# Kernel optimization log

Hardware: AMD Instinct MI355X
Metric: run time of the kernel (lower is better)

## Reference

```python
import jax, jax.numpy as jnp
import numpy as np

# ---- static config (matches init_kwargs) ----
B, N, DIM = 1, 2048, 1024
H, KVH, D = 16, 8, 64
GQ = H // KVH                 # grouped queries per kv head
WS = 64                       # sliding window size (causal, exact)
CBS, STRIDE = 32, 16          # compress block size / sliding stride
SEL_BLK, NSEL, NMEM = 32, 4, 1
NCB = N // STRIDE             # num compressed blocks (128)
NFB = N // SEL_BLK            # num fine blocks (64)
NCPF = SEL_BLK // STRIDE      # compressed blocks per fine block (2)
HID = CBS * D                 # compress MLP hidden (expand factor 1.0)
SCALE = D ** -0.5
THETA = 10000.0
NEG = -jnp.finfo(jnp.float32).max


def setup_inputs():
    key = jax.random.key(0)
    ks = jax.random.split(key, 16)
    s = 0.02
    r = lambda i, shape: jax.random.normal(ks[i], shape, jnp.float32) * s
    return {
        "inp": jax.random.normal(ks[0], (B, N, DIM), jnp.float32),
        "norm_g": jnp.ones((DIM,), jnp.float32),
        "Wqkv": r(1, (DIM, (H + 2 * KVH) * D)),
        "mem_kv": r(2, (2, KVH, NMEM, D)),
        "k_pos": r(3, (KVH, CBS, D)),
        "v_pos": r(4, (KVH, CBS, D)),
        "kW1": r(5, (CBS * D, HID)), "kb1": jnp.zeros((HID,), jnp.float32),
        "kW2": r(6, (HID, D)), "kb2": jnp.zeros((D,), jnp.float32),
        "vW1": r(7, (CBS * D, HID)), "vb1": jnp.zeros((HID,), jnp.float32),
        "vW2": r(8, (HID, D)), "vb2": jnp.zeros((D,), jnp.float32),
        "combW": r(9, (DIM, 3 * H)),
        "combB": jnp.tile(jnp.array([-2.0, -2.0, 2.0], jnp.float32), H),
        "Wout": r(10, (H * D, DIM)),
    }


def _rope(t):
    # lucidrains rotary-embedding-torch: interleaved adjacent-pair rotation
    inv_freq = 1.0 / (THETA ** (jnp.arange(0, D, 2, dtype=jnp.float32) / D))
    ang = jnp.arange(N, dtype=jnp.float32)[:, None] * inv_freq        # [N, D/2]
    cos = jnp.repeat(jnp.cos(ang), 2, axis=-1)                        # [N, D]
    sin = jnp.repeat(jnp.sin(ang), 2, axis=-1)
    t2 = t.reshape(*t.shape[:-1], D // 2, 2)
    rot = jnp.stack([-t2[..., 1], t2[..., 0]], axis=-1).reshape(t.shape)
    return t * cos + rot * sin


def _forward(inp, norm_g, Wqkv, mem_kv, k_pos, v_pos,
             kW1, kb1, kW2, kb2, vW1, vb1, vW2, vb2,
             combW, combB, Wout):
    # RMSNorm
    x = inp * jax.lax.rsqrt(jnp.mean(inp * inp, -1, keepdims=True)
                            + jnp.finfo(inp.dtype).eps) * norm_g
    qkv = x @ Wqkv
    q, k, v = jnp.split(qkv, [H * D, H * D + KVH * D], axis=-1)
    q = q.reshape(B, N, H, D).transpose(0, 2, 1, 3)      # b h n d
    k = k.reshape(B, N, KVH, D).transpose(0, 2, 1, 3)    # b kvh n d
    v = v.reshape(B, N, KVH, D).transpose(0, 2, 1, 3)

    # ---- compressed branch (overlapping windows, left zero pad) ----
    overlap = CBS - STRIDE
    kp = jnp.pad(k, ((0, 0), (0, 0), (overlap, 0), (0, 0)))
    vp = jnp.pad(v, ((0, 0), (0, 0), (overlap, 0), (0, 0)))
    widx = jnp.arange(NCB)[:, None] * STRIDE + jnp.arange(CBS)[None, :]  # [NCB, CBS]
    kw = kp[:, :, widx] + k_pos[None, :, None]   # b kvh w cbs d
    vw = vp[:, :, widx] + v_pos[None, :, None]

    def cmlp(t, W1, b1, W2, b2):
        t = t.reshape(B, KVH, NCB, CBS * D)
        return jax.nn.relu(t @ W1 + b1) @ W2 + b2       # b kvh w d

    ck = cmlp(kw, kW1, kb1, kW2, kb2)
    cv = cmlp(vw, vW1, vb1, vW2, vb2)
    ck = jnp.concatenate([jnp.broadcast_to(mem_kv[0], (B, KVH, NMEM, D)), ck], 2)
    cv = jnp.concatenate([jnp.broadcast_to(mem_kv[1], (B, KVH, NMEM, D)), cv], 2)

    qg = q.reshape(B, KVH, GQ, N, D)
    csim = jnp.einsum('bhgid,bhjd->bhgij', qg, ck) * SCALE   # no mask (cmask=None)
    cattn = jax.nn.softmax(csim, -1)
    cout = jnp.einsum('bhgij,bhjd->bhgid', cattn, cv).reshape(B, H, N, D)

    # rotary AFTER compressed attention (as in source)
    rq, rk = _rope(q), _rope(k)

    # ---- importance scores -> top-k fine block selection ----
    imp = csim[..., NMEM:].mean(2)                          # b kvh n NCB (share grouped q)
    imp = imp.reshape(B, KVH, N, NFB, NCPF).mean(-1)        # mean-pool to fine blocks
    q_blk = jnp.arange(N) // SEL_BLK
    diag = q_blk[:, None] == jnp.arange(NFB)[None, :]
    imp = jnp.where(diag[None, None], NEG, imp)             # mask own (diagonal) block
    imp = jax.nn.softmax(jnp.pad(imp, ((0, 0),) * 3 + ((1, 0),),
                                 constant_values=-1000.0), -1)[..., 1:]
    sel_val, sel_idx = jax.lax.top_k(imp, NSEL)             # b kvh n NSEL

    # ---- fine (block-selected) attention ----
    own = jnp.broadcast_to(q_blk[None, None, :, None], (B, KVH, N, 1))
    sel_idx = jnp.concatenate([sel_idx, own], -1)           # append own block
    fmask = jnp.repeat((sel_val > 1e-10)[..., None], SEL_BLK, -1)  # b kvh n NSEL blk
    causal_row = jnp.tril(jnp.ones((SEL_BLK, SEL_BLK), bool))[jnp.arange(N) % SEL_BLK]
    causal = jnp.broadcast_to(causal_row[None, None, :, None, :],
                              (B, KVH, N, 1, SEL_BLK))
    fmask = jnp.concatenate([fmask, causal], 3).reshape(B, KVH, N, (NSEL + 1) * SEL_BLK)

    fk_blocks = rk.reshape(B, KVH, NFB, SEL_BLK, D)
    fv_blocks = v.reshape(B, KVH, NFB, SEL_BLK, D)
    gather = jax.vmap(jax.vmap(lambda blocks, idx: blocks[idx]))  # over b, kvh
    fk = gather(fk_blocks, sel_idx).reshape(B, KVH, N, (NSEL + 1) * SEL_BLK, D)
    fv = gather(fv_blocks, sel_idx).reshape(B, KVH, N, (NSEL + 1) * SEL_BLK, D)

    rqg = rq.reshape(B, KVH, GQ, N, D)
    fsim = jnp.einsum('bhgid,bhijd->bhgij', rqg, fk) * SCALE
    fsim = jnp.where(fmask[:, :, None], fsim, NEG / 10)
    fattn = jax.nn.softmax(fsim, -1)
    fout = jnp.einsum('bhgij,bhijd->bhgid', fattn, fv).reshape(B, H, N, D)

    # ---- sliding window (causal, exact window size WS) ----
    NW = N // WS
    kp2 = jnp.pad(rk, ((0, 0), (0, 0), (WS, 0), (0, 0)))
    vp2 = jnp.pad(v, ((0, 0), (0, 0), (WS, 0), (0, 0)))
    kidx = jnp.arange(NW)[:, None] * WS + jnp.arange(2 * WS)[None, :]
    kwin = kp2[:, :, kidx]                                  # b kvh nw 2ws d
    vwin = vp2[:, :, kidx]
    qwin = rqg.reshape(B, KVH, GQ, NW, WS, D)
    ssim = jnp.einsum('bhgwid,bhwjd->bhgwij', qwin, kwin) * SCALE
    i = jnp.arange(WS)[:, None]
    j = jnp.arange(2 * WS)[None, :]
    diff = i - (j - WS)
    local_ok = (diff >= 0) & (diff < WS)                    # [WS, 2WS]
    keypos = jnp.arange(NW)[:, None, None] * WS + (jnp.arange(2 * WS) - WS)[None, None, :]
    smask = local_ok[None] & (keypos >= 0)                  # [NW, WS, 2WS]
    ssim = jnp.where(smask[None, None, None], ssim, NEG)
    sattn = jax.nn.softmax(ssim, -1)
    sout = jnp.einsum('bhgwij,bhwjd->bhgwid', sattn, vwin).reshape(B, H, N, D)

    # ---- learned strategy combination (compressed, fine, sliding) ----
    gates = jax.nn.sigmoid(x @ combW + combB).reshape(B, N, H, 3).transpose(0, 2, 1, 3)
    out = gates[..., 0:1] * cout + gates[..., 1:2] * fout + gates[..., 2:3] * sout
    out = out.transpose(0, 2, 1, 3).reshape(B, N, H * D) @ Wout
    return out


def reference(inp, norm_g, Wqkv, mem_kv, k_pos, v_pos,
              kW1, kb1, kW2, kb2, vW1, vb1, vW2, vb2,
              combW, combB, Wout):
    return _forward(inp, norm_g, Wqkv, mem_kv, k_pos, v_pos,
                    kW1, kb1, kW2, kb2, vW1, vb1, vW2, vb2,
                    combW, combB, Wout)
```

## Files before the change

### kernel.cpp

```cpp
#include <hip/hip_runtime.h>
#include <hip/hip_bf16.h>

#define NTOK 2048
#define DIM 1024
#define NH 16
#define KVH 8
#define GQ 2
#define HD 64
#define WS 64
#define CBS 32
#define STRIDE 16
#define SEL_BLK 32
#define NSEL 4
#define NMEM 1
#define NCB 128
#define NFB 64
#define HIDN 2048
#define SCALE 0.125f
#define NEGF (-3.4028234663852886e38f)
#define NEG10F (-3.4028234663852886e37f)

typedef __attribute__((ext_vector_type(8))) short bf16x8;
typedef __attribute__((ext_vector_type(4))) float f32x4;

__device__ __forceinline__ float bflo(unsigned u) { return __uint_as_float(u << 16); }
__device__ __forceinline__ float bfhi(unsigned u) { return __uint_as_float(u & 0xffff0000u); }
__device__ __forceinline__ void dot8(const float4& qa, const float4& qb, uint4 a, float& s) {
    s += qa.x * bflo(a.x) + qa.y * bfhi(a.x) + qa.z * bflo(a.y) + qa.w * bfhi(a.y) +
         qb.x * bflo(a.z) + qb.y * bfhi(a.z) + qb.z * bflo(a.w) + qb.w * bfhi(a.w);
}

__device__ __forceinline__ void gload_lds16(const void* g, void* l) {
    __builtin_amdgcn_global_load_lds((const __attribute__((address_space(1))) unsigned*)g,
                                     (__attribute__((address_space(3))) unsigned*)l, 16, 0, 0);
}

__device__ __forceinline__ void rms_body(const float* __restrict__ inp,
                                         const float* __restrict__ g,
                                         float* __restrict__ x,
                                         __hip_bfloat16* __restrict__ xb, int n) {
    const float* row = inp + (size_t)n * DIM;
    float ss = 0.f;
    for (int c = threadIdx.x; c < DIM; c += 256) { float v = row[c]; ss += v * v; }
    __shared__ float red[4];
    for (int o = 32; o; o >>= 1) ss += __shfl_down(ss, o, 64);
    if ((threadIdx.x & 63) == 0) red[threadIdx.x >> 6] = ss;
    __syncthreads();
    if (threadIdx.x == 0) red[0] = red[0] + red[1] + red[2] + red[3];
    __syncthreads();
    float rs = 1.0f / sqrtf(red[0] / (float)DIM + 1.1920928955078125e-07f);
    float* xr = x + (size_t)n * DIM;
    __hip_bfloat16* xbr = xb + (size_t)n * DIM;
    for (int c = threadIdx.x; c < DIM; c += 256) {
        float v = row[c] * rs * g[c];
        xr[c] = v;
        xbr[c] = __float2bfloat16(v);
    }
}

__device__ __forceinline__ void transpose_body(const float* __restrict__ B,
                                               __hip_bfloat16* __restrict__ Bt,
                                               int K, int N, int bx, int by) {
    __shared__ float tile[32][33];
    int n0 = bx * 32, k0 = by * 32;
    int x = threadIdx.x & 31, y = threadIdx.x >> 5;
    for (int i = 0; i < 4; i++) {
        int k = k0 + y + 8 * i, n = n0 + x;
        tile[y + 8 * i][x] = (k < K && n < N) ? B[(size_t)k * N + n] : 0.f;
    }
    __syncthreads();
    for (int i = 0; i < 4; i++) {
        int n = n0 + y + 8 * i, k = k0 + x;
        if (n < N && k < K) Bt[(size_t)n * K + k] = __float2bfloat16(tile[x][y + 8 * i]);
    }
}

__global__ __launch_bounds__(256) void pre_kernel(
    const float* inp, const float* norm_g, float* x, __hip_bfloat16* xb,
    const float* Wqkv, __hip_bfloat16* Wqkvt,
    const float* kW1, __hip_bfloat16* kW1t,
    const float* vW1, __hip_bfloat16* vW1t,
    const float* Wout, __hip_bfloat16* Woutt,
    const float* combW, __hip_bfloat16* combWt,
    const float* kW2, __hip_bfloat16* kW2t,
    const float* vW2, __hip_bfloat16* vW2t,
    const float* combB, float* gatesb,
    const float* kb2, float* ckraw,
    const float* vb2, float* cvraw) {
    int b = blockIdx.x;
    if (b < 2048) { rms_body(inp, norm_g, x, xb, b); return; }
    b -= 2048;
    if (b < 2048) { transpose_body(Wqkv, Wqkvt, 1024, 2048, b % 64, b / 64); return; }
    b -= 2048;
    if (b < 4096) { transpose_body(kW1, kW1t, 2048, 2048, b % 64, b / 64); return; }
    b -= 4096;
    if (b < 4096) { transpose_body(vW1, vW1t, 2048, 2048, b % 64, b / 64); return; }
    b -= 4096;
    if (b < 1024) { transpose_body(Wout, Woutt, 1024, 1024, b % 32, b / 32); return; }
    b -= 1024;
    if (b < 64) { transpose_body(combW, combWt, 1024, 48, b % 2, b / 2); return; }
    b -= 64;
    if (b < 128) { transpose_body(kW2, kW2t, 2048, 64, b % 2, b / 2); return; }
    b -= 128;
    if (b < 128) { transpose_body(vW2, vW2t, 2048, 64, b % 2, b / 2); return; }
    b -= 128;
    if (b < 384) {
        int idx = b * 256 + threadIdx.x;
        if (idx < 2048 * 48) gatesb[idx] = combB[idx % 48];
        return;
    }
    b -= 384;
    {
        int idx = b * 256 + threadIdx.x;
        int tot = 1024 * 64;
        if (idx < tot) ckraw[idx] = kb2[idx % 64];
        else if (idx < 2 * tot) { idx -= tot; cvraw[idx] = vb2[idx % 64]; }
        return;
    }
}
#define PRE_BLOCKS (2048 + 2048 + 4096 + 4096 + 1024 + 64 + 128 + 128 + 384 + 512)

template <int ACT, int OUTBF16>
__device__ __forceinline__ void mfma_gemm_body(const __hip_bfloat16* __restrict__ A,
                                               const __hip_bfloat16* __restrict__ Bt,
                                               const float* __restrict__ bias,
                                               void* __restrict__ Cp,
                                               int M, int N, int K, int bx, int by) {
    __shared__ __align__(16) short As[128 * 32];
    __shared__ __align__(16) short Bs[128 * 32];
    int tid = threadIdx.x;
    int lane = tid & 63, wave = tid >> 6;
    int wm = (wave >> 1) * 64, wn = (wave & 1) * 64;
    int m0 = by * 128, n0 = bx * 128;
    f32x4 acc[4][4];
    for (int r = 0; r < 4; r++)
        for (int c = 0; c < 4; c++)
            acc[r][c] = (f32x4){0.f, 0.f, 0.f, 0.f};

    int r0 = tid >> 2, kc0 = (tid & 3) * 8;
    int r1 = r0 + 64;

    for (int k0 = 0; k0 < K; k0 += 32) {
        __syncthreads();
        gload_lds16(A + (size_t)(m0 + r0) * K + k0 + kc0, &As[r0 * 32 + kc0]);
        gload_lds16(A + (size_t)(m0 + r1) * K + k0 + kc0, &As[r1 * 32 + kc0]);
        gload_lds16(Bt + (size_t)(n0 + r0) * K + k0 + kc0, &Bs[r0 * 32 + kc0]);
        gload_lds16(Bt + (size_t)(n0 + r1) * K + k0 + kc0, &Bs[r1 * 32 + kc0]);
        __syncthreads();
        bf16x8 af[4], bfr[4];
#pragma unroll
        for (int r = 0; r < 4; r++)
            af[r] = *(const bf16x8*)&As[(wm + r * 16 + (lane & 15)) * 32 + (lane >> 4) * 8];
#pragma unroll
        for (int c = 0; c < 4; c++)
            bfr[c] = *(const bf16x8*)&Bs[(wn + c * 16 + (lane & 15)) * 32 + (lane >> 4) * 8];
#pragma unroll
        for (int r = 0; r < 4; r++)
#pragma unroll
            for (int c = 0; c < 4; c++)
                acc[r][c] = __builtin_amdgcn_mfma_f32_16x16x32_bf16(af[r], bfr[c], acc[r][c], 0, 0, 0);
    }
    for (int r = 0; r < 4; r++) {
        int grow = m0 + wm + r * 16 + (lane >> 4) * 4;
        for (int c = 0; c < 4; c++) {
            int gcol = n0 + wn + c * 16 + (lane & 15);
            float bv = bias ? bias[gcol] : 0.f;
#pragma unroll
            for (int v = 0; v < 4; v++) {
                float val = acc[r][c][v] + bv;
                if (ACT == 1) val = fmaxf(val, 0.f);
                if (OUTBF16)
                    ((__hip_bfloat16*)Cp)[(size_t)(grow + v) * N + gcol] = __float2bfloat16(val);
                else
                    ((float*)Cp)[(size_t)(grow + v) * N + gcol] = val;
            }
        }
    }
}

template <int ACT, int OUTBF16>
__global__ __launch_bounds__(256) void mfma_gemm(const __hip_bfloat16* __restrict__ A,
                                                 const __hip_bfloat16* __restrict__ Bt,
                                                 const float* __restrict__ bias,
                                                 void* __restrict__ Cp,
                                                 int M, int N, int K) {
    mfma_gemm_body<ACT, OUTBF16>(A, Bt, bias, Cp, M, N, K, blockIdx.x, blockIdx.y);
}

__global__ __launch_bounds__(256) void mfma_gemm_pair(const __hip_bfloat16* A0,
                                                      const __hip_bfloat16* A1,
                                                      const __hip_bfloat16* Bt0,
                                                      const __hip_bfloat16* Bt1,
                                                      const float* bias0, const float* bias1,
                                                      __hip_bfloat16* C0, __hip_bfloat16* C1,
                                                      int M, int N, int K) {
    if (blockIdx.z == 0)
        mfma_gemm_body<1, 1>(A0, Bt0, bias0, C0, M, N, K, blockIdx.x, blockIdx.y);
    else
        mfma_gemm_body<1, 1>(A1, Bt1, bias1, C1, M, N, K, blockIdx.x, blockIdx.y);
}

__device__ __forceinline__ void skgemm_body(const __hip_bfloat16* __restrict__ A,
                                            const __hip_bfloat16* __restrict__ Bt,
                                            float* __restrict__ C,
                                            int M, int Nout, int K, int by, int bz, int nz) {
    __shared__ __align__(16) short As2[128 * 32];
    __shared__ __align__(16) short Bs2[64 * 32];
    int tid = threadIdx.x;
    int lane = tid & 63, wave = tid >> 6;
    int m0 = by * 128;
    int wm = wave * 32;
    int kchunk = K / nz;
    int kbase = bz * kchunk;
    f32x4 acc[2][4];
    for (int r = 0; r < 2; r++)
        for (int c = 0; c < 4; c++) acc[r][c] = (f32x4){0.f, 0.f, 0.f, 0.f};

    int ra = tid >> 2, kc = (tid & 3) * 8;
    int rb = ra < Nout ? ra : Nout - 1;
    for (int k0 = kbase; k0 < kbase + kchunk; k0 += 32) {
        __syncthreads();
        gload_lds16(A + (size_t)(m0 + ra) * K + k0 + kc, &As2[ra * 32 + kc]);
        gload_lds16(A + (size_t)(m0 + ra + 64) * K + k0 + kc, &As2[(ra + 64) * 32 + kc]);
        gload_lds16(Bt + (size_t)rb * K + k0 + kc, &Bs2[ra * 32 + kc]);
        __syncthreads();
        bf16x8 af[2], bfr[4];
#pragma unroll
        for (int r = 0; r < 2; r++)
            af[r] = *(const bf16x8*)&As2[(wm + r * 16 + (lane & 15)) * 32 + (lane >> 4) * 8];
#pragma unroll
        for (int c = 0; c < 4; c++)
            bfr[c] = *(const bf16x8*)&Bs2[(c * 16 + (lane & 15)) * 32 + (lane >> 4) * 8];
#pragma unroll
        for (int r = 0; r < 2; r++)
#pragma unroll
            for (int c = 0; c < 4; c++)
                acc[r][c] = __builtin_amdgcn_mfma_f32_16x16x32_bf16(af[r], bfr[c], acc[r][c], 0, 0, 0);
    }
    for (int r = 0; r < 2; r++) {
        int grow = m0 + wm + r * 16 + (lane >> 4) * 4;
        for (int c = 0; c < 4; c++) {
            int gcol = c * 16 + (lane & 15);
            if (gcol >= Nout) continue;
#pragma unroll
            for (int v = 0; v < 4; v++)
                atomicAdd(&C[(size_t)(grow + v) * Nout + gcol], acc[r][c][v]);
        }
    }
}

__global__ __launch_bounds__(256) void qkv_gates_kernel(const __hip_bfloat16* xb,
                                                        const __hip_bfloat16* Wqkvt,
                                                        float* qkv,
                                                        const __hip_bfloat16* combWt,
                                                        float* gatesb) {
    int b = blockIdx.x;
    if (b < 256) {
        mfma_gemm_body<0, 0>(xb, Wqkvt, nullptr, qkv, 2048, 2048, 1024, b & 15, b >> 4);
    } else {
        int s = b - 256;
        skgemm_body(xb, combWt, gatesb, 2048, 48, 1024, s & 15, s >> 4, 4);
    }
}

__global__ __launch_bounds__(256) void skgemm_pair(const __hip_bfloat16* A0,
                                                   const __hip_bfloat16* A1,
                                                   const __hip_bfloat16* Bt0,
                                                   const __hip_bfloat16* Bt1,
                                                   float* C0, float* C1,
                                                   int M, int Nout, int K) {
    if (blockIdx.x == 0)
        skgemm_body(A0, Bt0, C0, M, Nout, K, blockIdx.y, blockIdx.z, gridDim.z);
    else
        skgemm_body(A1, Bt1, C1, M, Nout, K, blockIdx.y, blockIdx.z, gridDim.z);
}

__global__ __launch_bounds__(256) void winrope_kernel(const float* __restrict__ qkv,
                                                      const float* __restrict__ k_pos,
                                                      const float* __restrict__ v_pos,
                                                      __hip_bfloat16* __restrict__ kwflat,
                                                      __hip_bfloat16* __restrict__ vwflat,
                                                      float* __restrict__ rq,
                                                      __hip_bfloat16* __restrict__ rk,
                                                      __hip_bfloat16* __restrict__ vt) {
    int b = blockIdx.x;
    int t = threadIdx.x;
    if (b < 4096) {
        size_t total = (size_t)(KVH * NCB) * HIDN;
        for (size_t e = (size_t)b * 256 + t; e < total; e += (size_t)4096 * 256) {
            int r = (int)(e >> 11);
            int c = (int)(e & 2047);
            int j = c >> 6, d = c & 63;
            int h = r >> 7, i = r & 127;
            int p = i * STRIDE + j - (CBS - STRIDE);
            float kb = k_pos[((size_t)h * CBS + j) * HD + d];
            float vb = v_pos[((size_t)h * CBS + j) * HD + d];
            float kv = 0.f, vv = 0.f;
            if (p >= 0) {
                kv = qkv[(size_t)p * 2048 + 1024 + h * HD + d];
                vv = qkv[(size_t)p * 2048 + 1536 + h * HD + d];
            }
            kwflat[e] = __float2bfloat16(kv + kb);
            vwflat[e] = __float2bfloat16(vv + vb);
        }
        return;
    }
    int n = b - 4096;
    for (int idx = t; idx < NH * 32; idx += 256) {
        int h = idx >> 5, f = idx & 31;
        float inv = exp2f((float)f * -0.41524101186092f);
        float ang = (float)n * inv;
        float cc = cosf(ang), ssn = sinf(ang);
        float a = qkv[(size_t)n * 2048 + h * HD + 2 * f];
        float bq = qkv[(size_t)n * 2048 + h * HD + 2 * f + 1];
        float* o = rq + ((size_t)h * NTOK + n) * HD + 2 * f;
        o[0] = a * cc - bq * ssn;
        o[1] = bq * cc + a * ssn;
    }
    for (int idx = t; idx < KVH * 32; idx += 256) {
        int h = idx >> 5, f = idx & 31;
        float inv = exp2f((float)f * -0.41524101186092f);
        float ang = (float)n * inv;
        float cc = cosf(ang), ssn = sinf(ang);
        float a = qkv[(size_t)n * 2048 + 1024 + h * HD + 2 * f];
        float bq = qkv[(size_t)n * 2048 + 1024 + h * HD + 2 * f + 1];
        __hip_bfloat16* o = rk + ((size_t)h * NTOK + n) * HD + 2 * f;
        o[0] = __float2bfloat16(a * cc - bq * ssn);
        o[1] = __float2bfloat16(bq * cc + a * ssn);
    }
    for (int idx = t; idx < KVH * HD; idx += 256) {
        int h = idx >> 6, d = idx & 63;
        vt[((size_t)h * NTOK + n) * HD + d] =
            __float2bfloat16(qkv[(size_t)n * 2048 + 1536 + h * HD + d]);
    }
}

__global__ __launch_bounds__(256) void cattn2_kernel(const float* __restrict__ qkv,
                                                     const float* __restrict__ ckraw,
                                                     const float* __restrict__ cvraw,
                                                     const float* __restrict__ memkv,
                                                     float* __restrict__ cout,
                                                     int* __restrict__ selidx,
                                                     int* __restrict__ selmask) {
    int h = blockIdx.x >> 6;
    int i0 = (blockIdx.x & 63) * 32;
    int t = threadIdx.x;
    __shared__ float qs[64][68];
    __shared__ float sc[64][132];
    __shared__ float scratch[32 * 68];
    __shared__ float memk[64], memv[64];

    for (int idx = t; idx < 4096; idx += 256) {
        int row = idx >> 6, d = idx & 63;
        int g = row >> 5, qi = row & 31;
        qs[row][d] = qkv[(size_t)(i0 + qi) * 2048 + (h * 2 + g) * 64 + d];
    }
    if (t < 64) { memk[t] = memkv[h * 64 + t]; memv[t] = memkv[(8 + h) * 64 + t]; }
    __syncthreads();
    if (t < 64) {
        float s = 0.f;
        for (int d = 0; d < 64; d++) s += qs[t][d] * memk[d];
        sc[t][0] = s * SCALE;
    }
    int rg = t >> 3, kg = t & 7;
    for (int c = 0; c < 4; c++) {
        __syncthreads();
        for (int idx = t; idx < 2048; idx += 256) {
            int jj = idx >> 6, d = idx & 63;
            scratch[jj * 68 + d] = ckraw[((size_t)h * 128 + c * 32 + jj) * 64 + d];
        }
        __syncthreads();
        float a0[4] = {}, a1[4] = {};
        for (int d = 0; d < 64; d += 4) {
            float4 q0 = *(const float4*)&qs[rg * 2][d];
            float4 q1 = *(const float4*)&qs[rg * 2 + 1][d];
#pragma unroll
            for (int kk = 0; kk < 4; kk++) {
                float4 kv = *(const float4*)&scratch[(kg + kk * 8) * 68 + d];
                a0[kk] += q0.x * kv.x + q0.y * kv.y + q0.z * kv.z + q0.w * kv.w;
                a1[kk] += q1.x * kv.x + q1.y * kv.y + q1.z * kv.z + q1.w * kv.w;
            }
        }
#pragma unroll
        for (int kk = 0; kk < 4; kk++) {
            sc[rg * 2][1 + c * 32 + kg + kk * 8] = a0[kk] * SCALE;
            sc[rg * 2 + 1][1 + c * 32 + kg + kk * 8] = a1[kk] * SCALE;
        }
    }
    __syncthreads();
    for (int idx = t; idx < 2048; idx += 256) {
        int qi = idx >> 6, fb = idx & 63;
        float v = 0.25f * (sc[qi][1 + 2 * fb] + sc[qi][2 + 2 * fb] +
                           sc[32 + qi][1 + 2 * fb] + sc[32 + qi][2 + 2 * fb]);
        if (fb == ((i0 + qi) >> 5)) v = NEGF;
        scratch[qi * 66 + fb] = v;
    }
    __syncthreads();
    if (t < 32) {
        float* row = &scratch[t * 66];
        float m = -1000.f;
        for (int j = 0; j < 64; j++) m = fmaxf(m, row[j]);
        float den = __expf(-1000.f - m);
        for (int j = 0; j < 64; j++) den += __expf(row[j] - m);
        float invd = 1.f / den;
        unsigned long long taken = 0ull;
        int mk = 0;
        size_t base = ((size_t)h * NTOK + i0 + t) * 5;
        for (int p = 0; p < NSEL; p++) {
            float bv = NEGF;
            int bi = 0;
            for (int j = 0; j < 64; j++) {
                if (!((taken >> j) & 1ull) && row[j] > bv) { bv = row[j]; bi = j; }
            }
            taken |= 1ull << bi;
            selidx[base + p] = bi;
            if (__expf(bv - m) * invd > 1e-10f) mk |= 1 << p;
        }
        selidx[base + 4] = (i0 + t) >> 5;
        selmask[h * NTOK + i0 + t] = mk;
    } else if (t >= 64 && t < 128) {
        int r = t - 64;
        float m = NEGF;
        for (int j = 0; j < 129; j++) m = fmaxf(m, sc[r][j]);
        float den = 0.f;
        for (int j = 0; j < 129; j++) { float e = __expf(sc[r][j] - m); sc[r][j] = e; den += e; }
        float inv = 1.f / den;
        for (int j = 0; j < 129; j++) sc[r][j] *= inv;
    }
    __syncthreads();
    int dg = t & 7;
    float o0[8], o1[8];
    {
        float p0 = sc[rg * 2][0], p1 = sc[rg * 2 + 1][0];
#pragma unroll
        for (int dd = 0; dd < 8; dd++) {
            float v = memv[dg + dd * 8];
            o0[dd] = p0 * v;
            o1[dd] = p1 * v;
        }
    }
    for (int c = 0; c < 4; c++) {
        __syncthreads();
        for (int idx = t; idx < 2048; idx += 256) {
            int jj = idx >> 6, d = idx & 63;
            scratch[jj * 68 + d] = cvraw[((size_t)h * 128 + c * 32 + jj) * 64 + d];
        }
        __syncthreads();
        for (int jj = 0; jj < 32; jj++) {
            float p0 = sc[rg * 2][1 + c * 32 + jj];
            float p1 = sc[rg * 2 + 1][1 + c * 32 + jj];
#pragma unroll
            for (int dd = 0; dd < 8; dd++) {
                float v = scratch[jj * 68 + dg + dd * 8];
                o0[dd] += p0 * v;
                o1[dd] += p1 * v;
            }
        }
    }
    {
        int row = rg * 2;
        int g = row >> 5, qi = row & 31;
        int g2 = (row + 1) >> 5, qi2 = (row + 1) & 31;
#pragma unroll
        for (int dd = 0; dd < 8; dd++) {
            cout[(((size_t)(h * 2 + g)) * NTOK + i0 + qi) * 64 + dd * 8 + dg] = o0[dd];
            cout[(((size_t)(h * 2 + g2)) * NTOK + i0 + qi2) * 64 + dd * 8 + dg] = o1[dd];
        }
    }
}

#define SLIDE_BLKS 1024
#define SROWS 79
#define SPAD 72
#define SLIDE_LDS (SROWS * SPAD * 2 * 2 + 4 * 128 * 4)
__global__ __launch_bounds__(256) void attn_fused4_kernel(const float* __restrict__ rq,
                                                          const __hip_bfloat16* __restrict__ rk,
                                                          const __hip_bfloat16* __restrict__ vt,
                                                          const int* __restrict__ selidx,
                                                          const int* __restrict__ selmask,
                                                          float* __restrict__ fout,
                                                          float* __restrict__ sout) {
    int tid = threadIdx.x;
    int ws = tid >> 6, lane = tid & 63;
    __shared__ __align__(16) char smem[SLIDE_LDS];

    int kq = lane >> 2, c = lane & 3;
    int kv8 = lane >> 3, c8 = lane & 7;

    if (blockIdx.x < SLIDE_BLKS) {
        int h = blockIdx.x & 7;
        int q0 = (int)(blockIdx.x >> 3) * 16;
        short* ks = (short*)smem;
        short* vs = ks + SROWS * SPAD;
        float* ps = (float*)(smem + SROWS * SPAD * 2 * 2);
        int basek = q0 - 63;
        for (int idx = tid; idx < SROWS * 8; idx += 256) {
            int row = idx >> 3, ch = (idx & 7) * 8;
            int kpos = basek + row;
            uint4 kv = (uint4){0u, 0u, 0u, 0u}, vv = (uint4){0u, 0u, 0u, 0u};
            if (kpos >= 0) {
                kv = *(const uint4*)(rk + ((size_t)h * NTOK + kpos) * 64 + ch);
                vv = *(const uint4*)(vt + ((size_t)h * NTOK + kpos) * 64 + ch);
            }
            *(uint4*)&ks[row * SPAD + ch] = kv;
            *(uint4*)&vs[row * SPAD + ch] = vv;
        }
        __syncthreads();
        float* p0 = ps + ws * 128;
        float* p1 = p0 + 64;
#pragma unroll 1
        for (int tq = 0; tq < 4; tq++) {
            int ibase = ws * 4 + tq;
            int i = q0 + ibase;
            const float* q0p = rq + ((size_t)(h * 2 + 0) * NTOK + i) * 64 + c * 16;
            const float* q1p = rq + ((size_t)(h * 2 + 1) * NTOK + i) * 64 + c * 16;
            float4 qa[4], qb[4];
#pragma unroll
            for (int u = 0; u < 4; u++) {
                qa[u] = *(const float4*)(q0p + u * 4);
                qb[u] = *(const float4*)(q1p + u * 4);
            }
#pragma unroll
            for (int kt = 0; kt < 4; kt++) {
                int key = kt * 16 + kq;
                const short* kr = &ks[(ibase + key) * SPAD + c * 16];
                float s0 = 0.f, s1 = 0.f;
                uint4 a = *(const uint4*)(kr);
                uint4 b = *(const uint4*)(kr + 8);
                dot8(qa[0], qa[1], a, s0); dot8(qa[2], qa[3], b, s0);
                dot8(qb[0], qb[1], a, s1); dot8(qb[2], qb[3], b, s1);
                s0 += __shfl_xor(s0, 1); s0 += __shfl_xor(s0, 2);
                s1 += __shfl_xor(s1, 1); s1 += __shfl_xor(s1, 2);
                int kpos = i - 63 + key;
                if (c == 0) {
                    p0[key] = (kpos >= 0) ? s0 * SCALE : NEG10F;
                    p1[key] = (kpos >= 0) ? s1 * SCALE : NEG10F;
                }
            }
            {
                float a0 = p0[lane], a1 = p1[lane];
                float m0 = a0, m1 = a1;
#pragma unroll
                for (int o = 1; o < 64; o <<= 1) {
                    m0 = fmaxf(m0, __shfl_xor(m0, o));
                    m1 = fmaxf(m1, __shfl_xor(m1, o));
                }
                float e0 = __expf(a0 - m0), e1 = __expf(a1 - m1);
                float d0 = e0, d1 = e1;
#pragma unroll
                for (int o = 1; o < 64; o <<= 1) {
                    d0 += __shfl_xor(d0, o);
                    d1 += __shfl_xor(d1, o);
                }
                p0[lane] = e0 / d0;
                p1[lane] = e1 / d1;
            }
            float o0[8] = {}, o1[8] = {};
#pragma unroll
            for (int pass = 0; pass < 8; pass++) {
                int j = pass * 8 + kv8;
                uint4 v = *(const uint4*)&vs[(ibase + j) * SPAD + c8 * 8];
                float pa = p0[j], pb = p1[j];
                float e0 = bflo(v.x), e1 = bfhi(v.x), e2 = bflo(v.y), e3 = bfhi(v.y);
                float e4 = bflo(v.z), e5 = bfhi(v.z), e6 = bflo(v.w), e7 = bfhi(v.w);
                o0[0] = fmaf(pa, e0, o0[0]); o0[1] = fmaf(pa, e1, o0[1]);
                o0[2] = fmaf(pa, e2, o0[2]); o0[3] = fmaf(pa, e3, o0[3]);
                o0[4] = fmaf(pa, e4, o0[4]); o0[5] = fmaf(pa, e5, o0[5]);
                o0[6] = fmaf(pa, e6, o0[6]); o0[7] = fmaf(pa, e7, o0[7]);
                o1[0] = fmaf(pb, e0, o1[0]); o1[1] = fmaf(pb, e1, o1[1]);
                o1[2] = fmaf(pb, e2, o1[2]); o1[3] = fmaf(pb, e3, o1[3]);
                o1[4] = fmaf(pb, e4, o1[4]); o1[5] = fmaf(pb, e5, o1[5]);
                o1[6] = fmaf(pb, e6, o1[6]); o1[7] = fmaf(pb, e7, o1[7]);
            }
#pragma unroll
            for (int o = 8; o <= 32; o <<= 1)
#pragma unroll
                for (int d = 0; d < 8; d++) {
                    o0[d] += __shfl_xor(o0[d], o);
                    o1[d] += __shfl_xor(o1[d], o);
                }
            if (kv8 == 0) {
                float* s0p = sout + ((size_t)(h * 2 + 0) * NTOK + i) * 64 + c8 * 8;
                float* s1p = sout + ((size_t)(h * 2 + 1) * NTOK + i) * 64 + c8 * 8;
                *(float4*)(s0p) = (float4){o0[0], o0[1], o0[2], o0[3]};
                *(float4*)(s0p + 4) = (float4){o0[4], o0[5], o0[6], o0[7]};
                *(float4*)(s1p) = (float4){o1[0], o1[1], o1[2], o1[3]};
                *(float4*)(s1p + 4) = (float4){o1[4], o1[5], o1[6], o1[7]};
            }
        }
    } else {
        int bb = blockIdx.x - SLIDE_BLKS;
        int h = bb & 7;
        int i = (bb >> 3) * 4 + ws;
        float* pbuf = (float*)smem;
        float* pf0 = pbuf + ws * 320;
        float* pf1 = pf0 + 160;

        size_t sbase = ((size_t)h * NTOK + i) * 5;
        int selr[5];
#pragma unroll
        for (int s = 0; s < 5; s++) selr[s] = selidx[sbase + s];
        int mk = selmask[h * NTOK + i];

        const float* q0p = rq + ((size_t)(h * 2 + 0) * NTOK + i) * 64 + c * 16;
        const float* q1p = rq + ((size_t)(h * 2 + 1) * NTOK + i) * 64 + c * 16;
        float4 q0[4], q1[4];
#pragma unroll
        for (int u = 0; u < 4; u++) {
            q0[u] = *(const float4*)(q0p + u * 4);
            q1[u] = *(const float4*)(q1p + u * 4);
        }
        int iq = i & 31;

#pragma unroll
        for (int kt = 0; kt < 10; kt++) {
            int slot = kt >> 1;
            int blk = selr[slot];
            int key = kt * 16 + kq;
            int jj = key & 31;
            int kpos = blk * 32 + jj;
            bool valid = (slot < 4) ? (((mk >> slot) & 1) != 0) : (jj <= iq);
            const __hip_bfloat16* kr = rk + ((size_t)h * NTOK + kpos) * 64 + c * 16;
            float s0 = 0.f, s1 = 0.f;
            uint4 a = *(const uint4*)(kr);
            uint4 b = *(const uint4*)(kr + 8);
            dot8(q0[0], q0[1], a, s0); dot8(q0[2], q0[3], b, s0);
            dot8(q1[0], q1[1], a, s1); dot8(q1[2], q1[3], b, s1);
            s0 += __shfl_xor(s0, 1); s0 += __shfl_xor(s0, 2);
            s1 += __shfl_xor(s1, 1); s1 += __shfl_xor(s1, 2);
            if (c == 0) {
                pf0[key] = valid ? s0 * SCALE : NEG10F;
                pf1[key] = valid ? s1 * SCALE : NEG10F;
            }
        }
        {
            float a0 = pf0[lane], b0 = pf0[lane + 64];
            float c0 = (lane < 32) ? pf0[lane + 128] : NEG10F;
            float a1 = pf1[lane], b1 = pf1[lane + 64];
            float c1 = (lane < 32) ? pf1[lane + 128] : NEG10F;
            float m0 = fmaxf(fmaxf(a0, b0), c0);
            float m1 = fmaxf(fmaxf(a1, b1), c1);
#pragma unroll
            for (int o = 1; o < 64; o <<= 1) {
                m0 = fmaxf(m0, __shfl_xor(m0, o));
                m1 = fmaxf(m1, __shfl_xor(m1, o));
            }
            float ea0 = __expf(a0 - m0), eb0 = __expf(b0 - m0), ec0 = (lane < 32) ? __expf(c0 - m0) : 0.f;
            float ea1 = __expf(a1 - m1), eb1 = __expf(b1 - m1), ec1 = (lane < 32) ? __expf(c1 - m1) : 0.f;
            float d0 = ea0 + eb0 + ec0;
            float d1 = ea1 + eb1 + ec1;
#pragma unroll
            for (int o = 1; o < 64; o <<= 1) {
                d0 += __shfl_xor(d0, o);
                d1 += __shfl_xor(d1, o);
            }
            float inv0 = 1.f / d0, inv1 = 1.f / d1;
            pf0[lane] = ea0 * inv0; pf0[lane + 64] = eb0 * inv0;
            pf1[lane] = ea1 * inv1; pf1[lane + 64] = eb1 * inv1;
            if (lane < 32) { pf0[lane + 128] = ec0 * inv0; pf1[lane + 128] = ec1 * inv1; }
        }
        float o0[8] = {}, o1[8] = {};
#pragma unroll
        for (int slot = 0; slot < 5; slot++) {
            const __hip_bfloat16* vbase = vt + ((size_t)h * NTOK + selr[slot] * 32) * 64;
#pragma unroll
            for (int pass = 0; pass < 4; pass++) {
                int j = pass * 8 + kv8;
                uint4 v = *(const uint4*)(vbase + j * 64 + c8 * 8);
                float pa = pf0[slot * 32 + j], pb = pf1[slot * 32 + j];
                float e0 = bflo(v.x), e1 = bfhi(v.x), e2 = bflo(v.y), e3 = bfhi(v.y);
                float e4 = bflo(v.z), e5 = bfhi(v.z), e6 = bflo(v.w), e7 = bfhi(v.w);
                o0[0] = fmaf(pa, e0, o0[0]); o0[1] = fmaf(pa, e1, o0[1]);
                o0[2] = fmaf(pa, e2, o0[2]); o0[3] = fmaf(pa, e3, o0[3]);
                o0[4] = fmaf(pa, e4, o0[4]); o0[5] = fmaf(pa, e5, o0[5]);
                o0[6] = fmaf(pa, e6, o0[6]); o0[7] = fmaf(pa, e7, o0[7]);
                o1[0] = fmaf(pb, e0, o1[0]); o1[1] = fmaf(pb, e1, o1[1]);
                o1[2] = fmaf(pb, e2, o1[2]); o1[3] = fmaf(pb, e3, o1[3]);
                o1[4] = fmaf(pb, e4, o1[4]); o1[5] = fmaf(pb, e5, o1[5]);
                o1[6] = fmaf(pb, e6, o1[6]); o1[7] = fmaf(pb, e7, o1[7]);
            }
        }
#pragma unroll
        for (int o = 8; o <= 32; o <<= 1)
#pragma unroll
            for (int d = 0; d < 8; d++) {
                o0[d] += __shfl_xor(o0[d], o);
                o1[d] += __shfl_xor(o1[d], o);
            }
        if (kv8 == 0) {
            float* f0 = fout + ((size_t)(h * 2 + 0) * NTOK + i) * 64 + c8 * 8;
            float* f1 = fout + ((size_t)(h * 2 + 1) * NTOK + i) * 64 + c8 * 8;
            *(float4*)(f0) = (float4){o0[0], o0[1], o0[2], o0[3]};
            *(float4*)(f0 + 4) = (float4){o0[4], o0[5], o0[6], o0[7]};
            *(float4*)(f1) = (float4){o1[0], o1[1], o1[2], o1[3]};
            *(float4*)(f1 + 4) = (float4){o1[4], o1[5], o1[6], o1[7]};
        }
    }
}

__global__ __launch_bounds__(256) void combine_kernel(const float* __restrict__ gateslin,
                                                      const float* __restrict__ cout,
                                                      const float* __restrict__ fout,
                                                      const float* __restrict__ sout,
                                                      __hip_bfloat16* __restrict__ att) {
    int n = blockIdx.x;
    for (int c = threadIdx.x; c < NH * HD; c += 256) {
        int hd = c >> 6, d = c & 63;
        float g0 = 1.f / (1.f + expf(-gateslin[(size_t)n * (NH * 3) + hd * 3 + 0]));
        float g1 = 1.f / (1.f + expf(-gateslin[(size_t)n * (NH * 3) + hd * 3 + 1]));
        float g2 = 1.f / (1.f + expf(-gateslin[(size_t)n * (NH * 3) + hd * 3 + 2]));
        size_t o = ((size_t)hd * NTOK + n) * HD + d;
        att[(size_t)n * (NH * HD) + c] =
            __float2bfloat16(g0 * cout[o] + g1 * fout[o] + g2 * sout[o]);
    }
}

extern "C" void kernel_launch(void* const* d_in, const int* in_sizes, int n_in,
                              void* d_out, int out_size, void* d_ws, size_t ws_size,
                              hipStream_t stream) {
    const float* inp    = (const float*)d_in[0];
    const float* norm_g = (const float*)d_in[1];
    const float* Wqkv   = (const float*)d_in[2];
    const float* mem_kv = (const float*)d_in[3];
    const float* k_pos  = (const float*)d_in[4];
    const float* v_pos  = (const float*)d_in[5];
    const float* kW1    = (const float*)d_in[6];
    const float* kb1    = (const float*)d_in[7];
    const float* kW2    = (const float*)d_in[8];
    const float* kb2    = (const float*)d_in[9];
    const float* vW1    = (const float*)d_in[10];
    const float* vb1    = (const float*)d_in[11];
    const float* vW2    = (const float*)d_in[12];
    const float* vb2    = (const float*)d_in[13];
    const float* combW  = (const float*)d_in[14];
    const float* combB  = (const float*)d_in[15];
    const float* Wout   = (const float*)d_in[16];
    float* out = (float*)d_out;

    char* base = (char*)d_ws;
    size_t off = 0;
    auto alloc = [&](size_t bytes) {
        void* p = base + off;
        off += (bytes + 255) & ~(size_t)255;
        return p;
    };
    float* x            = (float*)alloc((size_t)NTOK * DIM * 4);
    __hip_bfloat16* xb  = (__hip_bfloat16*)alloc((size_t)NTOK * DIM * 2);
    float* qkv          = (float*)alloc((size_t)NTOK * 2048 * 4);
    __hip_bfloat16* Wqkvt = (__hip_bfloat16*)alloc((size_t)2048 * 1024 * 2);
    __hip_bfloat16* kW1t  = (__hip_bfloat16*)alloc((size_t)2048 * 2048 * 2);
    __hip_bfloat16* vW1t  = (__hip_bfloat16*)alloc((size_t)2048 * 2048 * 2);
    __hip_bfloat16* Woutt = (__hip_bfloat16*)alloc((size_t)1024 * 1024 * 2);
    __hip_bfloat16* combWt = (__hip_bfloat16*)alloc((size_t)48 * 1024 * 2);
    __hip_bfloat16* kW2t  = (__hip_bfloat16*)alloc((size_t)64 * 2048 * 2);
    __hip_bfloat16* vW2t  = (__hip_bfloat16*)alloc((size_t)64 * 2048 * 2);
    __hip_bfloat16* kwflat = (__hip_bfloat16*)alloc((size_t)KVH * NCB * HIDN * 2);
    __hip_bfloat16* vwflat = (__hip_bfloat16*)alloc((size_t)KVH * NCB * HIDN * 2);
    __hip_bfloat16* hidkb = (__hip_bfloat16*)alloc((size_t)KVH * NCB * HIDN * 2);
    __hip_bfloat16* hidvb = (__hip_bfloat16*)alloc((size_t)KVH * NCB * HIDN * 2);
    float* ckraw        = (float*)alloc((size_t)KVH * NCB * HD * 4);
    float* cvraw        = (float*)alloc((size_t)KVH * NCB * HD * 4);
    float* rq           = (float*)alloc((size_t)NH * NTOK * HD * 4);
    __hip_bfloat16* rk  = (__hip_bfloat16*)alloc((size_t)KVH * NTOK * HD * 2);
    __hip_bfloat16* vt  = (__hip_bfloat16*)alloc((size_t)KVH * NTOK * HD * 2);
    float* coutb        = (float*)alloc((size_t)NH * NTOK * HD * 4);
    float* foutb        = (float*)alloc((size_t)NH * NTOK * HD * 4);
    float* soutb        = (float*)alloc((size_t)NH * NTOK * HD * 4);
    float* gatesb       = (float*)alloc((size_t)NTOK * NH * 3 * 4);
    __hip_bfloat16* attb = (__hip_bfloat16*)alloc((size_t)NTOK * DIM * 2);
    int* selidx         = (int*)alloc((size_t)KVH * NTOK * 5 * 4);
    int* selmask        = (int*)alloc((size_t)KVH * NTOK * 4);
    (void)ws_size; (void)in_sizes; (void)n_in; (void)out_size;

    pre_kernel<<<PRE_BLOCKS, 256, 0, stream>>>(inp, norm_g, x, xb,
                                               Wqkv, Wqkvt, kW1, kW1t, vW1, vW1t,
                                               Wout, Woutt, combW, combWt,
                                               kW2, kW2t, vW2, vW2t,
                                               combB, gatesb, kb2, ckraw, vb2, cvraw);
    qkv_gates_kernel<<<320, 256, 0, stream>>>(xb, Wqkvt, qkv, combWt, gatesb);
    winrope_kernel<<<4096 + 2048, 256, 0, stream>>>(qkv, k_pos, v_pos, kwflat, vwflat,
                                                    rq, rk, vt);
    mfma_gemm_pair<<<dim3(16, 8, 2), 256, 0, stream>>>(kwflat, vwflat, kW1t, vW1t,
                                                       kb1, vb1, hidkb, hidvb,
                                                       1024, 2048, 2048);
    skgemm_pair<<<dim3(2, 8, 8), 256, 0, stream>>>(hidkb, hidvb, kW2t, vW2t,
                                                   ckraw, cvraw, 1024, 64, 2048);
    cattn2_kernel<<<KVH * (NTOK / 32), 256, 0, stream>>>(qkv, ckraw, cvraw, mem_kv,
                                                         coutb, selidx, selmask);
    attn_fused4_kernel<<<SLIDE_BLKS + 4096, 256, 0, stream>>>(rq, rk, vt, selidx, selmask,
                                                              foutb, soutb);
    combine_kernel<<<NTOK, 256, 0, stream>>>(gatesb, coutb, foutb, soutb, attb);
    mfma_gemm<0, 0><<<dim3(8, 16), 256, 0, stream>>>(attb, Woutt, nullptr, out, 2048, 1024, 1024);
}
```

Measured before the change: 371.4 us.

## Shrink GEMM tiles to 128x64 and read sliding V directly from global

Every MFMA GEMM (QKV, compress MLP first layer, output projection) now uses a 128x64 tile instead of 128x128, with each wave covering 32 rows, which doubles the block count. The aim is better CU occupancy on a GPU with many CUs, in exchange for less operand reuse per block. In the sliding-window attention path, V is no longer staged in LDS; the PV loop reads it from global memory with clamped indices. This halves the LDS footprint but adds uncoalesced global loads inside the inner loop.

```diff
diff --git a/kernel.cpp b/kernel.cpp
--- a/kernel.cpp
+++ b/kernel.cpp
@@ -121,49 +121,45 @@
 #define PRE_BLOCKS (2048 + 2048 + 4096 + 4096 + 1024 + 64 + 128 + 128 + 384 + 512)
 
 template <int ACT, int OUTBF16>
-__device__ __forceinline__ void mfma_gemm_body(const __hip_bfloat16* __restrict__ A,
-                                               const __hip_bfloat16* __restrict__ Bt,
-                                               const float* __restrict__ bias,
-                                               void* __restrict__ Cp,
-                                               int M, int N, int K, int bx, int by) {
-    __shared__ __align__(16) short As[128 * 32];
-    __shared__ __align__(16) short Bs[128 * 32];
+__device__ __forceinline__ void gemm64_body(const __hip_bfloat16* __restrict__ A,
+                                            const __hip_bfloat16* __restrict__ Bt,
+                                            const float* __restrict__ bias,
+                                            void* __restrict__ Cp,
+                                            int M, int N, int K, int bx, int by) {
+    __shared__ __align__(16) short As2[128 * 32];
+    __shared__ __align__(16) short Bs2[64 * 32];
     int tid = threadIdx.x;
     int lane = tid & 63, wave = tid >> 6;
-    int wm = (wave >> 1) * 64, wn = (wave & 1) * 64;
-    int m0 = by * 128, n0 = bx * 128;
-    f32x4 acc[4][4];
-    for (int r = 0; r < 4; r++)
+    int m0 = by * 128, n0 = bx * 64;
+    int wm = wave * 32;
+    f32x4 acc[2][4];
+    for (int r = 0; r < 2; r++)
+        for (int c = 0; c < 4; c++) acc[r][c] = (f32x4){0.f, 0.f, 0.f, 0.f};
+
+    int ra = tid >> 2, kc = (tid & 3) * 8;
+    for (int k0 = 0; k0 < K; k0 += 32) {
+        __syncthreads();
+        gload_lds16(A + (size_t)(m0 + ra) * K + k0 + kc, &As2[ra * 32 + kc]);
+        gload_lds16(A + (size_t)(m0 + ra + 64) * K + k0 + kc, &As2[(ra + 64) * 32 + kc]);
+        gload_lds16(Bt + (size_t)(n0 + ra) * K + k0 + kc, &Bs2[ra * 32 + kc]);
+        __syncthreads();
+        bf16x8 af[2], bfr[4];
+#pragma unroll
+        for (int r = 0; r < 2; r++)
+            af[r] = *(const bf16x8*)&As2[(wm + r * 16 + (lane & 15)) * 32 + (lane >> 4) * 8];
+#pragma unroll
         for (int c = 0; c < 4; c++)
-            acc[r][c] = (f32x4){0.f, 0.f, 0.f, 0.f};
-
-    int r0 = tid >> 2, kc0 = (tid & 3) * 8;
-    int r1 = r0 + 64;
-
-    for (int k0 = 0; k0 < K; k0 += 32) {
-        __syncthreads();
-        gload_lds16(A + (size_t)(m0 + r0) * K + k0 + kc0, &As[r0 * 32 + kc0]);
-        gload_lds16(A + (size_t)(m0 + r1) * K + k0 + kc0, &As[r1 * 32 + kc0]);
-        gload_lds16(Bt + (size_t)(n0 + r0) * K + k0 + kc0, &Bs[r0 * 32 + kc0]);
-        gload_lds16(Bt + (size_t)(n0 + r1) * K + k0 + kc0, &Bs[r1 * 32 + kc0]);
-        __syncthreads();
-        bf16x8 af[4], bfr[4];
-#pragma unroll
-        for (int r = 0; r < 4; r++)
-            af[r] = *(const bf16x8*)&As[(wm + r * 16 + (lane & 15)) * 32 + (lane >> 4) * 8];
-#pragma unroll
-        for (int c = 0; c < 4; c++)
-            bfr[c] = *(const bf16x8*)&Bs[(wn + c * 16 + (lane & 15)) * 32 + (lane >> 4) * 8];
-#pragma unroll
-        for (int r = 0; r < 4; r++)
+            bfr[c] = *(const bf16x8*)&Bs2[(c * 16 + (lane & 15)) * 32 + (lane >> 4) * 8];
+#pragma unroll
+        for (int r = 0; r < 2; r++)
 #pragma unroll
             for (int c = 0; c < 4; c++)
                 acc[r][c] = __builtin_amdgcn_mfma_f32_16x16x32_bf16(af[r], bfr[c], acc[r][c], 0, 0, 0);
     }
-    for (int r = 0; r < 4; r++) {
+    for (int r = 0; r < 2; r++) {
         int grow = m0 + wm + r * 16 + (lane >> 4) * 4;
         for (int c = 0; c < 4; c++) {
-            int gcol = n0 + wn + c * 16 + (lane & 15);
+            int gcol = n0 + c * 16 + (lane & 15);
             float bv = bias ? bias[gcol] : 0.f;
 #pragma unroll
             for (int v = 0; v < 4; v++) {
@@ -179,25 +175,25 @@
 }
 
 template <int ACT, int OUTBF16>
-__global__ __launch_bounds__(256) void mfma_gemm(const __hip_bfloat16* __restrict__ A,
-                                                 const __hip_bfloat16* __restrict__ Bt,
-                                                 const float* __restrict__ bias,
-                                                 void* __restrict__ Cp,
-                                                 int M, int N, int K) {
-    mfma_gemm_body<ACT, OUTBF16>(A, Bt, bias, Cp, M, N, K, blockIdx.x, blockIdx.y);
-}
-
-__global__ __launch_bounds__(256) void mfma_gemm_pair(const __hip_bfloat16* A0,
-                                                      const __hip_bfloat16* A1,
-                                                      const __hip_bfloat16* Bt0,
-                                                      const __hip_bfloat16* Bt1,
-                                                      const float* bias0, const float* bias1,
-                                                      __hip_bfloat16* C0, __hip_bfloat16* C1,
-                                                      int M, int N, int K) {
+__global__ __launch_bounds__(256) void gemm64(const __hip_bfloat16* __restrict__ A,
+                                              const __hip_bfloat16* __restrict__ Bt,
+                                              const float* __restrict__ bias,
+                                              void* __restrict__ Cp,
+                                              int M, int N, int K) {
+    gemm64_body<ACT, OUTBF16>(A, Bt, bias, Cp, M, N, K, blockIdx.x, blockIdx.y);
+}
+
+__global__ __launch_bounds__(256) void gemm64_pair(const __hip_bfloat16* A0,
+                                                   const __hip_bfloat16* A1,
+                                                   const __hip_bfloat16* Bt0,
+                                                   const __hip_bfloat16* Bt1,
+                                                   const float* bias0, const float* bias1,
+                                                   __hip_bfloat16* C0, __hip_bfloat16* C1,
+                                                   int M, int N, int K) {
     if (blockIdx.z == 0)
-        mfma_gemm_body<1, 1>(A0, Bt0, bias0, C0, M, N, K, blockIdx.x, blockIdx.y);
+        gemm64_body<1, 1>(A0, Bt0, bias0, C0, M, N, K, blockIdx.x, blockIdx.y);
     else
-        mfma_gemm_body<1, 1>(A1, Bt1, bias1, C1, M, N, K, blockIdx.x, blockIdx.y);
+        gemm64_body<1, 1>(A1, Bt1, bias1, C1, M, N, K, blockIdx.x, blockIdx.y);
 }
 
 __device__ __forceinline__ void skgemm_body(const __hip_bfloat16* __restrict__ A,
@@ -255,10 +251,10 @@
                                                         const __hip_bfloat16* combWt,
                                                         float* gatesb) {
     int b = blockIdx.x;
-    if (b < 256) {
-        mfma_gemm_body<0, 0>(xb, Wqkvt, nullptr, qkv, 2048, 2048, 1024, b & 15, b >> 4);
+    if (b < 512) {
+        gemm64_body<0, 0>(xb, Wqkvt, nullptr, qkv, 2048, 2048, 1024, b & 31, b >> 5);
     } else {
-        int s = b - 256;
+        int s = b - 512;
         skgemm_body(xb, combWt, gatesb, 2048, 48, 1024, s & 15, s >> 4, 4);
     }
 }
@@ -472,8 +468,8 @@
 #define SLIDE_BLKS 1024
 #define SROWS 79
 #define SPAD 72
-#define SLIDE_LDS (SROWS * SPAD * 2 * 2 + 4 * 128 * 4)
-__global__ __launch_bounds__(256) void attn_fused4_kernel(const float* __restrict__ rq,
+#define SLIDE_LDS (SROWS * SPAD * 2 + 4 * 128 * 4)
+__global__ __launch_bounds__(256) void attn_fused6_kernel(const float* __restrict__ rq,
                                                           const __hip_bfloat16* __restrict__ rk,
                                                           const __hip_bfloat16* __restrict__ vt,
                                                           const int* __restrict__ selidx,
@@ -491,19 +487,15 @@
         int h = blockIdx.x & 7;
         int q0 = (int)(blockIdx.x >> 3) * 16;
         short* ks = (short*)smem;
-        short* vs = ks + SROWS * SPAD;
-        float* ps = (float*)(smem + SROWS * SPAD * 2 * 2);
+        float* ps = (float*)(smem + SROWS * SPAD * 2);
         int basek = q0 - 63;
         for (int idx = tid; idx < SROWS * 8; idx += 256) {
             int row = idx >> 3, ch = (idx & 7) * 8;
             int kpos = basek + row;
-            uint4 kv = (uint4){0u, 0u, 0u, 0u}, vv = (uint4){0u, 0u, 0u, 0u};
-            if (kpos >= 0) {
+            uint4 kv = (uint4){0u, 0u, 0u, 0u};
+            if (kpos >= 0)
                 kv = *(const uint4*)(rk + ((size_t)h * NTOK + kpos) * 64 + ch);
-                vv = *(const uint4*)(vt + ((size_t)h * NTOK + kpos) * 64 + ch);
-            }
             *(uint4*)&ks[row * SPAD + ch] = kv;
-            *(uint4*)&vs[row * SPAD + ch] = vv;
         }
         __syncthreads();
         float* p0 = ps + ws * 128;
@@ -559,7 +551,9 @@
 #pragma unroll
             for (int pass = 0; pass < 8; pass++) {
                 int j = pass * 8 + kv8;
-                uint4 v = *(const uint4*)&vs[(ibase + j) * SPAD + c8 * 8];
+                int kpos = i - 63 + j;
+                int kcl = kpos >= 0 ? kpos : 0;
+                uint4 v = *(const uint4*)(vt + ((size_t)h * NTOK + kcl) * 64 + c8 * 8);
                 float pa = p0[j], pb = p1[j];
                 float e0 = bflo(v.x), e1 = bfhi(v.x), e2 = bflo(v.y), e3 = bfhi(v.y);
                 float e4 = bflo(v.z), e5 = bfhi(v.z), e6 = bflo(v.w), e7 = bfhi(v.w);
@@ -777,18 +771,18 @@
                                                Wout, Woutt, combW, combWt,
                                                kW2, kW2t, vW2, vW2t,
                                                combB, gatesb, kb2, ckraw, vb2, cvraw);
-    qkv_gates_kernel<<<320, 256, 0, stream>>>(xb, Wqkvt, qkv, combWt, gatesb);
+    qkv_gates_kernel<<<576, 256, 0, stream>>>(xb, Wqkvt, qkv, combWt, gatesb);
     winrope_kernel<<<4096 + 2048, 256, 0, stream>>>(qkv, k_pos, v_pos, kwflat, vwflat,
                                                     rq, rk, vt);
-    mfma_gemm_pair<<<dim3(16, 8, 2), 256, 0, stream>>>(kwflat, vwflat, kW1t, vW1t,
-                                                       kb1, vb1, hidkb, hidvb,
-                                                       1024, 2048, 2048);
+    gemm64_pair<<<dim3(32, 8, 2), 256, 0, stream>>>(kwflat, vwflat, kW1t, vW1t,
+                                                    kb1, vb1, hidkb, hidvb,
+                                                    1024, 2048, 2048);
     skgemm_pair<<<dim3(2, 8, 8), 256, 0, stream>>>(hidkb, hidvb, kW2t, vW2t,
                                                    ckraw, cvraw, 1024, 64, 2048);
     cattn2_kernel<<<KVH * (NTOK / 32), 256, 0, stream>>>(qkv, ckraw, cvraw, mem_kv,
                                                          coutb, selidx, selmask);
-    attn_fused4_kernel<<<SLIDE_BLKS + 4096, 256, 0, stream>>>(rq, rk, vt, selidx, selmask,
+    attn_fused6_kernel<<<SLIDE_BLKS + 4096, 256, 0, stream>>>(rq, rk, vt, selidx, selmask,
                                                               foutb, soutb);
     combine_kernel<<<NTOK, 256, 0, stream>>>(gatesb, coutb, foutb, soutb, attb);
-    mfma_gemm<0, 0><<<dim3(8, 16), 256, 0, stream>>>(attb, Woutt, nullptr, out, 2048, 1024, 1024);
-}
+    gemm64<0, 0><<<dim3(16, 16), 256, 0, stream>>>(attb, Woutt, nullptr, out, 2048, 1024, 1024);
+}
```

Result: faster. 363.4 us (-2.2%).
